# Optimization experiments

Hardware: AMD Instinct MI355X
Metric: run time of the kernel (lower is better)

Reference implementation:

```python
import jax, jax.numpy as jnp
import numpy as np

N_NODES = 100000
N_EDGES = 1600000
IN_DIM = 128
OUT_DIM = 128


def setup_inputs() -> dict:
    key = jax.random.key(0)
    k_x, k_r, k_c, k_v, k_w, k_b = jax.random.split(key, 6)
    x = jax.random.normal(k_x, (N_NODES, IN_DIM), dtype=jnp.float32)
    rows = jax.random.randint(k_r, (N_EDGES,), 0, N_NODES, dtype=jnp.int32)
    cols = jax.random.randint(k_c, (N_EDGES,), 0, N_NODES, dtype=jnp.int32)
    vals = jax.random.uniform(k_v, (N_EDGES,), dtype=jnp.float32)
    # nn.Linear(in_dim, out_dim): kaiming-uniform-ish init, exact values irrelevant
    bound = 1.0 / np.sqrt(IN_DIM)
    W = jax.random.uniform(k_w, (IN_DIM, OUT_DIM), dtype=jnp.float32, minval=-bound, maxval=bound)
    b = jax.random.uniform(k_b, (OUT_DIM,), dtype=jnp.float32, minval=-bound, maxval=bound)
    return {"x": x, "W": W, "b": b, "vals": vals, "rows": rows, "cols": cols}


def reference(x, W, b, vals, rows, cols):
    # x = self.linear(x)
    h = x @ W + b  # [N, out_dim]
    # x = torch.sparse.mm(adj, x): out[r] += vals[e] * h[cols[e]] for each edge e with rows[e]==r
    msgs = vals[:, None] * h[cols]  # [E, out_dim]
    out = jax.ops.segment_sum(msgs, rows, num_segments=N_NODES)  # [N, out_dim]
    return out
```

## Files before the change

### kernel.cpp

```cpp
#include <hip/hip_runtime.h>

#define N_NODES 100000
#define N_EDGES 1600000
#define DIM 128
#define NBKT 391
#define B1   256
#define EPB  6250
#define CAP  4608

typedef __attribute__((ext_vector_type(8))) short bf16x8;
typedef __attribute__((ext_vector_type(4))) float f32x4;

__device__ __forceinline__ unsigned short f2bf(float f) {
    unsigned u = __float_as_uint(f);
    u += 0x7FFF + ((u >> 16) & 1);
    return (unsigned short)(u >> 16);
}
__device__ __forceinline__ float bflo(unsigned u) { return __uint_as_float(u << 16); }
__device__ __forceinline__ float bfhi(unsigned u) { return __uint_as_float(u & 0xFFFF0000u); }

__global__ __launch_bounds__(256) void wt_pack(const float* __restrict__ W,
                                               uint4* __restrict__ wtf) {
    const int t = blockIdx.x * 256 + threadIdx.x;
    const int f = t >> 6;
    const int l = t & 63;
    const int kc = f >> 3, nt = f & 7;
    const int quad = l >> 4, n = l & 15;
    unsigned o[4];
    #pragma unroll
    for (int jj = 0; jj < 4; ++jj) {
        const int k0 = kc * 32 + quad * 8 + jj * 2;
        const unsigned short lo = f2bf(W[(k0 + 0) * DIM + nt * 16 + n]);
        const unsigned short hi = f2bf(W[(k0 + 1) * DIM + nt * 16 + n]);
        o[jj] = (unsigned)lo | ((unsigned)hi << 16);
    }
    wtf[t] = make_uint4(o[0], o[1], o[2], o[3]);
}

__global__ __launch_bounds__(256) void gemm_mfma(const float* __restrict__ x,
                                                 const uint4* __restrict__ wtf,
                                                 const float* __restrict__ b,
                                                 unsigned short* __restrict__ h) {
    const int wave = threadIdx.x >> 6;
    const int lane = threadIdx.x & 63;
    const int quad = lane >> 4;
    const int m = lane & 15;
    const int row_base = blockIdx.x * 64 + wave * 16;
    const int row = row_base + m;
    const bool rok = (row < N_NODES);

    uint4 bf[32];
    #pragma unroll
    for (int f = 0; f < 32; ++f) bf[f] = wtf[f * 64 + lane];

    bf16x8 af[4];
    #pragma unroll
    for (int kc = 0; kc < 4; ++kc) {
        float4 v0, v1;
        if (rok) {
            v0 = *(const float4*)&x[(size_t)row * DIM + kc * 32 + quad * 8];
            v1 = *(const float4*)&x[(size_t)row * DIM + kc * 32 + quad * 8 + 4];
        } else {
            v0 = make_float4(0.f, 0.f, 0.f, 0.f);
            v1 = make_float4(0.f, 0.f, 0.f, 0.f);
        }
        union { bf16x8 v; unsigned u[4]; } a;
        a.u[0] = (unsigned)f2bf(v0.x) | ((unsigned)f2bf(v0.y) << 16);
        a.u[1] = (unsigned)f2bf(v0.z) | ((unsigned)f2bf(v0.w) << 16);
        a.u[2] = (unsigned)f2bf(v1.x) | ((unsigned)f2bf(v1.y) << 16);
        a.u[3] = (unsigned)f2bf(v1.z) | ((unsigned)f2bf(v1.w) << 16);
        af[kc] = a.v;
    }

    f32x4 acc[8];
    #pragma unroll
    for (int nt = 0; nt < 8; ++nt) {
        const float bv = b[nt * 16 + m];
        acc[nt] = (f32x4){bv, bv, bv, bv};
    }

    #pragma unroll
    for (int kc = 0; kc < 4; ++kc) {
        #pragma unroll
        for (int nt = 0; nt < 8; ++nt) {
            union { uint4 u; bf16x8 v; } bb; bb.u = bf[kc * 8 + nt];
            acc[nt] = __builtin_amdgcn_mfma_f32_16x16x32_bf16(af[kc], bb.v, acc[nt], 0, 0, 0);
        }
    }

    #pragma unroll
    for (int nt = 0; nt < 8; ++nt) {
        #pragma unroll
        for (int i = 0; i < 4; ++i) {
            const int r = row_base + quad * 4 + i;
            if (r < N_NODES) h[(size_t)r * DIM + nt * 16 + m] = f2bf(acc[nt][i]);
        }
    }
}

__global__ __launch_bounds__(256) void p1_count(const int* __restrict__ rows,
                                                int* __restrict__ cnt) {
    __shared__ int c[NBKT];
    const int k = blockIdx.x, t = threadIdx.x;
    for (int b = t; b < NBKT; b += 256) c[b] = 0;
    __syncthreads();
    const int e0 = k * EPB;
    #pragma unroll
    for (int i = 0; i < 6; ++i) {
        const int4 r4 = *(const int4*)&rows[e0 + (t + i * 256) * 4];
        atomicAdd(&c[r4.x >> 8], 1);
        atomicAdd(&c[r4.y >> 8], 1);
        atomicAdd(&c[r4.z >> 8], 1);
        atomicAdd(&c[r4.w >> 8], 1);
    }
    if (t < EPB - 6144) atomicAdd(&c[rows[e0 + 6144 + t] >> 8], 1);
    __syncthreads();
    for (int b = t; b < NBKT; b += 256) cnt[b * B1 + k] = c[b];
}

__global__ __launch_bounds__(512) void p1_scan_buckets(const int* __restrict__ cnt,
                                                       int* __restrict__ bktbase) {
    __shared__ int s[512];
    const int t = threadIdx.x;
    int tot = 0;
    if (t < NBKT) {
        for (int k = 0; k < B1; ++k) tot += cnt[t * B1 + k];
    }
    s[t] = tot;
    __syncthreads();
    for (int o = 1; o < 512; o <<= 1) {
        const int add = (t >= o) ? s[t - o] : 0;
        __syncthreads();
        s[t] += add;
        __syncthreads();
    }
    if (t < NBKT) bktbase[t] = s[t] - tot;
    if (t == NBKT - 1) bktbase[NBKT] = s[t];
}

__global__ __launch_bounds__(256) void p1_scan_blocks(const int* __restrict__ cnt,
                                                      const int* __restrict__ bktbase,
                                                      int* __restrict__ offs) {
    __shared__ int s[256];
    const int b = blockIdx.x, t = threadIdx.x;
    const int v = cnt[b * B1 + t];
    s[t] = v;
    __syncthreads();
    for (int o = 1; o < 256; o <<= 1) {
        const int add = (t >= o) ? s[t - o] : 0;
        __syncthreads();
        s[t] += add;
        __syncthreads();
    }
    offs[b * B1 + t] = bktbase[b] + s[t] - v;
}

__global__ __launch_bounds__(256) void p1_scatter(const int* __restrict__ rows,
                                                  const int* __restrict__ cols,
                                                  const float* __restrict__ vals,
                                                  const int* __restrict__ offs,
                                                  int2* __restrict__ binned) {
    __shared__ int cur[NBKT];
    const int k = blockIdx.x, t = threadIdx.x;
    for (int b = t; b < NBKT; b += 256) cur[b] = offs[b * B1 + k];
    __syncthreads();
    const int e0 = k * EPB;
    #pragma unroll
    for (int i = 0; i < 6; ++i) {
        const int g = (t + i * 256) * 4;
        const int4   r4 = *(const int4*)&rows[e0 + g];
        const int4   c4 = *(const int4*)&cols[e0 + g];
        const float4 v4 = *(const float4*)&vals[e0 + g];
        int p;
        p = atomicAdd(&cur[r4.x >> 8], 1);
        binned[p] = make_int2(((r4.x & 255) << 24) | c4.x, __float_as_int(v4.x));
        p = atomicAdd(&cur[r4.y >> 8], 1);
        binned[p] = make_int2(((r4.y & 255) << 24) | c4.y, __float_as_int(v4.y));
        p = atomicAdd(&cur[r4.z >> 8], 1);
        binned[p] = make_int2(((r4.z & 255) << 24) | c4.z, __float_as_int(v4.z));
        p = atomicAdd(&cur[r4.w >> 8], 1);
        binned[p] = make_int2(((r4.w & 255) << 24) | c4.w, __float_as_int(v4.w));
    }
    if (t < EPB - 6144) {
        const int e = e0 + 6144 + t;
        const int r = rows[e];
        const int p = atomicAdd(&cur[r >> 8], 1);
        binned[p] = make_int2(((r & 255) << 24) | cols[e], __float_as_int(vals[e]));
    }
    __syncthreads();
}

__global__ __launch_bounds__(512, 6) void p2_gather(const unsigned* __restrict__ h32,
                                                    const int2* __restrict__ binned,
                                                    const int* __restrict__ bktbase,
                                                    float* __restrict__ out) {
    __shared__ int2 ebuf[CAP];
    __shared__ int rcount[256], rstart[256], rcur[256], sscan[256];
    const int b = blockIdx.x, t = threadIdx.x;
    const int s0 = bktbase[b];
    const int n = bktbase[b + 1] - s0;

    int2 ereg[9];
    int nm = 0;
    #pragma unroll
    for (int jj = 0; jj < 9; ++jj) {
        const int j = t + jj * 512;
        if (j < n) { ereg[jj] = binned[s0 + j]; nm = jj + 1; }
    }

    if (t < 256) rcount[t] = 0;
    __syncthreads();
    #pragma unroll
    for (int jj = 0; jj < 9; ++jj)
        if (jj < nm) atomicAdd(&rcount[((unsigned)ereg[jj].x) >> 24], 1);
    __syncthreads();

    if (t < 256) sscan[t] = rcount[t];
    __syncthreads();
    for (int o = 1; o < 256; o <<= 1) {
        const int add = (t < 256 && t >= o) ? sscan[t - o] : 0;
        __syncthreads();
        if (t < 256) sscan[t] += add;
        __syncthreads();
    }
    if (t < 256) { rstart[t] = sscan[t] - rcount[t]; rcur[t] = sscan[t] - rcount[t]; }
    __syncthreads();

    #pragma unroll
    for (int jj = 0; jj < 9; ++jj)
        if (jj < nm) {
            const int lr = ((unsigned)ereg[jj].x) >> 24;
            const int pos = atomicAdd(&rcur[lr], 1);
            ebuf[pos] = make_int2(ereg[jj].x & 0x00FFFFFF, ereg[jj].y);
        }
    __syncthreads();

    const int wave = t >> 6, lane = t & 63;
    const char* hbase = (const char*)h32;
    const unsigned lane4 = (unsigned)lane * 4u;

    for (int i = 0; i < 16; ++i) {
        const int lr0 = wave * 32 + i;
        const int lr1 = lr0 + 16;
        const int r0 = b * 256 + lr0;
        const int r1 = b * 256 + lr1;
        const int st0 = rstart[lr0], cn0 = rcount[lr0];
        const int st1 = rstart[lr1], cn1 = rcount[lr1];

        float a0x = 0.f, a0y = 0.f, c0x = 0.f, c0y = 0.f;
        float a1x = 0.f, a1y = 0.f, c1x = 0.f, c1y = 0.f;
        int j0 = 0, j1 = 0;

        while (j0 + 2 <= cn0 && j1 + 2 <= cn1) {
            const int2 e0 = ebuf[st0 + j0], e1 = ebuf[st0 + j0 + 1];
            const int2 f0 = ebuf[st1 + j1], f1 = ebuf[st1 + j1 + 1];
            const unsigned u0 = *(const unsigned*)(hbase + ((((unsigned)e0.x) << 8) | lane4));
            const unsigned u1 = *(const unsigned*)(hbase + ((((unsigned)e1.x) << 8) | lane4));
            const unsigned w0 = *(const unsigned*)(hbase + ((((unsigned)f0.x) << 8) | lane4));
            const unsigned w1 = *(const unsigned*)(hbase + ((((unsigned)f1.x) << 8) | lane4));
            const float v0 = __int_as_float(e0.y), v1 = __int_as_float(e1.y);
            const float s0v = __int_as_float(f0.y), s1v = __int_as_float(f1.y);
            a0x = fmaf(v0, bflo(u0), a0x);  a0y = fmaf(v0, bfhi(u0), a0y);
            c0x = fmaf(v1, bflo(u1), c0x);  c0y = fmaf(v1, bfhi(u1), c0y);
            a1x = fmaf(s0v, bflo(w0), a1x); a1y = fmaf(s0v, bfhi(w0), a1y);
            c1x = fmaf(s1v, bflo(w1), c1x); c1y = fmaf(s1v, bfhi(w1), c1y);
            j0 += 2; j1 += 2;
        }
        for (; j0 + 2 <= cn0; j0 += 2) {
            const int2 e0 = ebuf[st0 + j0], e1 = ebuf[st0 + j0 + 1];
            const unsigned u0 = *(const unsigned*)(hbase + ((((unsigned)e0.x) << 8) | lane4));
            const unsigned u1 = *(const unsigned*)(hbase + ((((unsigned)e1.x) << 8) | lane4));
            const float v0 = __int_as_float(e0.y), v1 = __int_as_float(e1.y);
            a0x = fmaf(v0, bflo(u0), a0x); a0y = fmaf(v0, bfhi(u0), a0y);
            c0x = fmaf(v1, bflo(u1), c0x); c0y = fmaf(v1, bfhi(u1), c0y);
        }
        if (j0 < cn0) {
            const int2 e0 = ebuf[st0 + j0];
            const unsigned u0 = *(const unsigned*)(hbase + ((((unsigned)e0.x) << 8) | lane4));
            const float v0 = __int_as_float(e0.y);
            a0x = fmaf(v0, bflo(u0), a0x); a0y = fmaf(v0, bfhi(u0), a0y);
        }
        for (; j1 + 2 <= cn1; j1 += 2) {
            const int2 f0 = ebuf[st1 + j1], f1 = ebuf[st1 + j1 + 1];
            const unsigned w0 = *(const unsigned*)(hbase + ((((unsigned)f0.x) << 8) | lane4));
            const unsigned w1 = *(const unsigned*)(hbase + ((((unsigned)f1.x) << 8) | lane4));
            const float s0v = __int_as_float(f0.y), s1v = __int_as_float(f1.y);
            a1x = fmaf(s0v, bflo(w0), a1x); a1y = fmaf(s0v, bfhi(w0), a1y);
            c1x = fmaf(s1v, bflo(w1), c1x); c1y = fmaf(s1v, bfhi(w1), c1y);
        }
        if (j1 < cn1) {
            const int2 f0 = ebuf[st1 + j1];
            const unsigned w0 = *(const unsigned*)(hbase + ((((unsigned)f0.x) << 8) | lane4));
            const float s0v = __int_as_float(f0.y);
            a1x = fmaf(s0v, bflo(w0), a1x); a1y = fmaf(s0v, bfhi(w0), a1y);
        }

        if (r0 < N_NODES) {
            float2 o; o.x = a0x + c0x; o.y = a0y + c0y;
            *(float2*)&out[(size_t)r0 * DIM + lane * 2] = o;
        }
        if (r1 < N_NODES) {
            float2 o; o.x = a1x + c1x; o.y = a1y + c1y;
            *(float2*)&out[(size_t)r1 * DIM + lane * 2] = o;
        }
    }
}

extern "C" void kernel_launch(void* const* d_in, const int* in_sizes, int n_in,
                              void* d_out, int out_size, void* d_ws, size_t ws_size,
                              hipStream_t stream) {
    const float* x    = (const float*)d_in[0];
    const float* W    = (const float*)d_in[1];
    const float* b    = (const float*)d_in[2];
    const float* vals = (const float*)d_in[3];
    const int*   rows = (const int*)d_in[4];
    const int*   cols = (const int*)d_in[5];
    float* out = (float*)d_out;

    char* ws = (char*)d_ws;
    unsigned short* h = (unsigned short*)(ws + 0);
    uint4* wtf    = (uint4*)(ws + 25600000);
    int*   cnt    = (int*)  (ws + 25632768);
    int*   offs   = (int*)  (ws + 26033152);
    int*   bktbase= (int*)  (ws + 26433536);
    int2*  binned = (int2*) (ws + 26435104);

    wt_pack<<<8, 256, 0, stream>>>(W, wtf);
    gemm_mfma<<<(N_NODES + 63) / 64, 256, 0, stream>>>(x, wtf, b, h);

    p1_count<<<B1, 256, 0, stream>>>(rows, cnt);
    p1_scan_buckets<<<1, 512, 0, stream>>>(cnt, bktbase);
    p1_scan_blocks<<<NBKT, 256, 0, stream>>>(cnt, bktbase, offs);
    p1_scatter<<<B1, 256, 0, stream>>>(rows, cols, vals, offs, binned);

    p2_gather<<<NBKT, 512, 0, stream>>>((const unsigned*)h, binned, bktbase, out);
}
```

Measured before the change: 252.5 us.

## Fuse GEMM with bucket counting, halve bucket size, stage GEMM output in LDS

The bucket-count pass now runs as extra blocks inside the GEMM launch, so the two independent jobs overlap and one launch is dropped. Buckets shrink from 256 to 128 rows, giving 782 gather blocks with smaller LDS buffers and fewer per-thread registers, which should raise occupancy and load balance in the gather. The GEMM output is staged through shared memory so h is written as coalesced 16-byte stores instead of scattered 2-byte ones. The single-block serial bucket total is replaced by a parallel reduction kernel plus a 1024-thread scan, at the cost of one more launch.

```diff
diff --git a/kernel.cpp b/kernel.cpp
--- a/kernel.cpp
+++ b/kernel.cpp
@@ -3,10 +3,11 @@
 #define N_NODES 100000
 #define N_EDGES 1600000
 #define DIM 128
-#define NBKT 391
+#define NBKT 782
 #define B1   256
 #define EPB  6250
-#define CAP  4608
+#define CAP  2560
+#define GEMM_NB 1563
 
 typedef __attribute__((ext_vector_type(8))) short bf16x8;
 typedef __attribute__((ext_vector_type(4))) float f32x4;
@@ -37,10 +38,34 @@
     wtf[t] = make_uint4(o[0], o[1], o[2], o[3]);
 }
 
-__global__ __launch_bounds__(256) void gemm_mfma(const float* __restrict__ x,
-                                                 const uint4* __restrict__ wtf,
-                                                 const float* __restrict__ b,
-                                                 unsigned short* __restrict__ h) {
+#define ROWSTRIDE 136
+__global__ __launch_bounds__(256) void gemm_count(const float* __restrict__ x,
+                                                  const uint4* __restrict__ wtf,
+                                                  const float* __restrict__ b,
+                                                  unsigned short* __restrict__ h,
+                                                  const int* __restrict__ rows,
+                                                  int* __restrict__ cnt) {
+    __shared__ uint4 smem4[4 * 16 * ROWSTRIDE / 8];
+    if (blockIdx.x >= GEMM_NB) {
+        int* c = (int*)smem4;
+        const int k = blockIdx.x - GEMM_NB, t = threadIdx.x;
+        for (int bb = t; bb < NBKT; bb += 256) c[bb] = 0;
+        __syncthreads();
+        const int e0 = k * EPB;
+        #pragma unroll
+        for (int i = 0; i < 6; ++i) {
+            const int4 r4 = *(const int4*)&rows[e0 + (t + i * 256) * 4];
+            atomicAdd(&c[r4.x >> 7], 1);
+            atomicAdd(&c[r4.y >> 7], 1);
+            atomicAdd(&c[r4.z >> 7], 1);
+            atomicAdd(&c[r4.w >> 7], 1);
+        }
+        if (t < EPB - 6144) atomicAdd(&c[rows[e0 + 6144 + t] >> 7], 1);
+        __syncthreads();
+        for (int bb = t; bb < NBKT; bb += 256) cnt[bb * B1 + k] = c[bb];
+        return;
+    }
+
     const int wave = threadIdx.x >> 6;
     const int lane = threadIdx.x & 63;
     const int quad = lane >> 4;
@@ -88,53 +113,52 @@
         }
     }
 
+    unsigned short* sh = (unsigned short*)smem4 + wave * 16 * ROWSTRIDE;
     #pragma unroll
     for (int nt = 0; nt < 8; ++nt) {
         #pragma unroll
-        for (int i = 0; i < 4; ++i) {
-            const int r = row_base + quad * 4 + i;
-            if (r < N_NODES) h[(size_t)r * DIM + nt * 16 + m] = f2bf(acc[nt][i]);
-        }
-    }
-}
-
-__global__ __launch_bounds__(256) void p1_count(const int* __restrict__ rows,
-                                                int* __restrict__ cnt) {
-    __shared__ int c[NBKT];
-    const int k = blockIdx.x, t = threadIdx.x;
-    for (int b = t; b < NBKT; b += 256) c[b] = 0;
-    __syncthreads();
-    const int e0 = k * EPB;
-    #pragma unroll
-    for (int i = 0; i < 6; ++i) {
-        const int4 r4 = *(const int4*)&rows[e0 + (t + i * 256) * 4];
-        atomicAdd(&c[r4.x >> 8], 1);
-        atomicAdd(&c[r4.y >> 8], 1);
-        atomicAdd(&c[r4.z >> 8], 1);
-        atomicAdd(&c[r4.w >> 8], 1);
-    }
-    if (t < EPB - 6144) atomicAdd(&c[rows[e0 + 6144 + t] >> 8], 1);
-    __syncthreads();
-    for (int b = t; b < NBKT; b += 256) cnt[b * B1 + k] = c[b];
-}
-
-__global__ __launch_bounds__(512) void p1_scan_buckets(const int* __restrict__ cnt,
-                                                       int* __restrict__ bktbase) {
-    __shared__ int s[512];
+        for (int i = 0; i < 4; ++i)
+            sh[(quad * 4 + i) * ROWSTRIDE + nt * 16 + m] = f2bf(acc[nt][i]);
+    }
+    __syncthreads();
+    uint4* hv4 = (uint4*)h;
+    const int seg = lane & 15;
+    #pragma unroll
+    for (int c = 0; c < 4; ++c) {
+        const int rl = (lane >> 4) + c * 4;
+        const int r = row_base + rl;
+        const uint4 v = *(const uint4*)&sh[rl * ROWSTRIDE + seg * 8];
+        if (r < N_NODES) hv4[(size_t)r * 16 + seg] = v;
+    }
+}
+
+__global__ __launch_bounds__(256) void p1_totals(const int* __restrict__ cnt,
+                                                 int* __restrict__ tot) {
+    __shared__ int s[256];
+    const int t = threadIdx.x, bb = blockIdx.x;
+    s[t] = cnt[bb * B1 + t];
+    __syncthreads();
+    for (int o = 128; o > 0; o >>= 1) {
+        if (t < o) s[t] += s[t + o];
+        __syncthreads();
+    }
+    if (t == 0) tot[bb] = s[0];
+}
+
+__global__ __launch_bounds__(1024) void p1_scan_tot(const int* __restrict__ tot,
+                                                    int* __restrict__ bktbase) {
+    __shared__ int s[1024];
     const int t = threadIdx.x;
-    int tot = 0;
-    if (t < NBKT) {
-        for (int k = 0; k < B1; ++k) tot += cnt[t * B1 + k];
-    }
-    s[t] = tot;
-    __syncthreads();
-    for (int o = 1; o < 512; o <<= 1) {
+    const int v = (t < NBKT) ? tot[t] : 0;
+    s[t] = v;
+    __syncthreads();
+    for (int o = 1; o < 1024; o <<= 1) {
         const int add = (t >= o) ? s[t - o] : 0;
         __syncthreads();
         s[t] += add;
         __syncthreads();
     }
-    if (t < NBKT) bktbase[t] = s[t] - tot;
+    if (t < NBKT) bktbase[t] = s[t] - v;
     if (t == NBKT - 1) bktbase[NBKT] = s[t];
 }
 
@@ -142,8 +166,8 @@
                                                       const int* __restrict__ bktbase,
                                                       int* __restrict__ offs) {
     __shared__ int s[256];
-    const int b = blockIdx.x, t = threadIdx.x;
-    const int v = cnt[b * B1 + t];
+    const int bb = blockIdx.x, t = threadIdx.x;
+    const int v = cnt[bb * B1 + t];
     s[t] = v;
     __syncthreads();
     for (int o = 1; o < 256; o <<= 1) {
@@ -152,7 +176,7 @@
         s[t] += add;
         __syncthreads();
     }
-    offs[b * B1 + t] = bktbase[b] + s[t] - v;
+    offs[bb * B1 + t] = bktbase[bb] + s[t] - v;
 }
 
 __global__ __launch_bounds__(256) void p1_scatter(const int* __restrict__ rows,
@@ -162,7 +186,7 @@
                                                   int2* __restrict__ binned) {
     __shared__ int cur[NBKT];
     const int k = blockIdx.x, t = threadIdx.x;
-    for (int b = t; b < NBKT; b += 256) cur[b] = offs[b * B1 + k];
+    for (int bb = t; bb < NBKT; bb += 256) cur[bb] = offs[bb * B1 + k];
     __syncthreads();
     const int e0 = k * EPB;
     #pragma unroll
@@ -172,62 +196,61 @@
         const int4   c4 = *(const int4*)&cols[e0 + g];
         const float4 v4 = *(const float4*)&vals[e0 + g];
         int p;
-        p = atomicAdd(&cur[r4.x >> 8], 1);
-        binned[p] = make_int2(((r4.x & 255) << 24) | c4.x, __float_as_int(v4.x));
-        p = atomicAdd(&cur[r4.y >> 8], 1);
-        binned[p] = make_int2(((r4.y & 255) << 24) | c4.y, __float_as_int(v4.y));
-        p = atomicAdd(&cur[r4.z >> 8], 1);
-        binned[p] = make_int2(((r4.z & 255) << 24) | c4.z, __float_as_int(v4.z));
-        p = atomicAdd(&cur[r4.w >> 8], 1);
-        binned[p] = make_int2(((r4.w & 255) << 24) | c4.w, __float_as_int(v4.w));
+        p = atomicAdd(&cur[r4.x >> 7], 1);
+        binned[p] = make_int2(((r4.x & 127) << 24) | c4.x, __float_as_int(v4.x));
+        p = atomicAdd(&cur[r4.y >> 7], 1);
+        binned[p] = make_int2(((r4.y & 127) << 24) | c4.y, __float_as_int(v4.y));
+        p = atomicAdd(&cur[r4.z >> 7], 1);
+        binned[p] = make_int2(((r4.z & 127) << 24) | c4.z, __float_as_int(v4.z));
+        p = atomicAdd(&cur[r4.w >> 7], 1);
+        binned[p] = make_int2(((r4.w & 127) << 24) | c4.w, __float_as_int(v4.w));
     }
     if (t < EPB - 6144) {
         const int e = e0 + 6144 + t;
         const int r = rows[e];
-        const int p = atomicAdd(&cur[r >> 8], 1);
-        binned[p] = make_int2(((r & 255) << 24) | cols[e], __float_as_int(vals[e]));
-    }
-    __syncthreads();
-}
-
-__global__ __launch_bounds__(512, 6) void p2_gather(const unsigned* __restrict__ h32,
-                                                    const int2* __restrict__ binned,
-                                                    const int* __restrict__ bktbase,
-                                                    float* __restrict__ out) {
+        const int p = atomicAdd(&cur[r >> 7], 1);
+        binned[p] = make_int2(((r & 127) << 24) | cols[e], __float_as_int(vals[e]));
+    }
+}
+
+__global__ __launch_bounds__(512) void p2_gather(const unsigned* __restrict__ h32,
+                                                 const int2* __restrict__ binned,
+                                                 const int* __restrict__ bktbase,
+                                                 float* __restrict__ out) {
     __shared__ int2 ebuf[CAP];
-    __shared__ int rcount[256], rstart[256], rcur[256], sscan[256];
+    __shared__ int rcount[128], rstart[128], rcur[128], sscan[128];
     const int b = blockIdx.x, t = threadIdx.x;
     const int s0 = bktbase[b];
     const int n = bktbase[b + 1] - s0;
 
-    int2 ereg[9];
+    int2 ereg[5];
     int nm = 0;
     #pragma unroll
-    for (int jj = 0; jj < 9; ++jj) {
+    for (int jj = 0; jj < 5; ++jj) {
         const int j = t + jj * 512;
         if (j < n) { ereg[jj] = binned[s0 + j]; nm = jj + 1; }
     }
 
-    if (t < 256) rcount[t] = 0;
-    __syncthreads();
-    #pragma unroll
-    for (int jj = 0; jj < 9; ++jj)
+    if (t < 128) rcount[t] = 0;
+    __syncthreads();
+    #pragma unroll
+    for (int jj = 0; jj < 5; ++jj)
         if (jj < nm) atomicAdd(&rcount[((unsigned)ereg[jj].x) >> 24], 1);
     __syncthreads();
 
-    if (t < 256) sscan[t] = rcount[t];
-    __syncthreads();
-    for (int o = 1; o < 256; o <<= 1) {
-        const int add = (t < 256 && t >= o) ? sscan[t - o] : 0;
-        __syncthreads();
-        if (t < 256) sscan[t] += add;
-        __syncthreads();
-    }
-    if (t < 256) { rstart[t] = sscan[t] - rcount[t]; rcur[t] = sscan[t] - rcount[t]; }
-    __syncthreads();
-
-    #pragma unroll
-    for (int jj = 0; jj < 9; ++jj)
+    if (t < 128) sscan[t] = rcount[t];
+    __syncthreads();
+    for (int o = 1; o < 128; o <<= 1) {
+        const int add = (t < 128 && t >= o) ? sscan[t - o] : 0;
+        __syncthreads();
+        if (t < 128) sscan[t] += add;
+        __syncthreads();
+    }
+    if (t < 128) { rstart[t] = sscan[t] - rcount[t]; rcur[t] = sscan[t] - rcount[t]; }
+    __syncthreads();
+
+    #pragma unroll
+    for (int jj = 0; jj < 5; ++jj)
         if (jj < nm) {
             const int lr = ((unsigned)ereg[jj].x) >> 24;
             const int pos = atomicAdd(&rcur[lr], 1);
@@ -239,11 +262,11 @@
     const char* hbase = (const char*)h32;
     const unsigned lane4 = (unsigned)lane * 4u;
 
-    for (int i = 0; i < 16; ++i) {
-        const int lr0 = wave * 32 + i;
-        const int lr1 = lr0 + 16;
-        const int r0 = b * 256 + lr0;
-        const int r1 = b * 256 + lr1;
+    for (int i = 0; i < 8; ++i) {
+        const int lr0 = wave * 16 + i;
+        const int lr1 = lr0 + 8;
+        const int r0 = b * 128 + lr0;
+        const int r1 = b * 128 + lr1;
         const int st0 = rstart[lr0], cn0 = rcount[lr0];
         const int st1 = rstart[lr1], cn1 = rcount[lr1];
 
@@ -321,16 +344,19 @@
     unsigned short* h = (unsigned short*)(ws + 0);
     uint4* wtf    = (uint4*)(ws + 25600000);
     int*   cnt    = (int*)  (ws + 25632768);
-    int*   offs   = (int*)  (ws + 26033152);
-    int*   bktbase= (int*)  (ws + 26433536);
-    int2*  binned = (int2*) (ws + 26435104);
+    int*   offs   = (int*)  (ws + 26433536);
+    int*   tot    = (int*)  (ws + 27234304);
+    int*   bktbase= (int*)  (ws + 27237440);
+    int2*  binned = (int2*) (ws + 27240576);
 
     wt_pack<<<8, 256, 0, stream>>>(W, wtf);
-    gemm_mfma<<<(N_NODES + 63) / 64, 256, 0, stream>>>(x, wtf, b, h);
-
-    p1_count<<<B1, 256, 0, stream>>>(rows, cnt);
-    p1_scan_buckets<<<1, 512, 0, stream>>>(cnt, bktbase);
+
+    gemm_count<<<GEMM_NB + B1, 256, 0, stream>>>(x, wtf, b, h, rows, cnt);
+
+    p1_totals<<<NBKT, 256, 0, stream>>>(cnt, tot);
+    p1_scan_tot<<<1, 1024, 0, stream>>>(tot, bktbase);
     p1_scan_blocks<<<NBKT, 256, 0, stream>>>(cnt, bktbase, offs);
+
     p1_scatter<<<B1, 256, 0, stream>>>(rows, cols, vals, offs, binned);
 
     p2_gather<<<NBKT, 512, 0, stream>>>((const unsigned*)h, binned, bktbase, out);
```

After: 230.5 us. -8.7%, faster.
